# Kernel tuning notes

Hardware: AMD Instinct MI355X
Metric: run time of the kernel (lower is better)

The kernel has to match this reference:

```python
import jax, jax.numpy as jnp
import numpy as np

B, N, FIN, H, D = 2, 512, 128, 4, 64
NEG_SLOPE = 0.2


def setup_inputs() -> dict:
    key = jax.random.key(0)
    ks = jax.random.split(key, 5)
    x = jax.random.normal(ks[0], (B, N, FIN), dtype=jnp.float32)
    # xavier-ish scaled params
    W_proj = jax.random.normal(ks[1], (H, FIN, D), dtype=jnp.float32) * (1.0 / np.sqrt(FIN + D))
    b_proj = jnp.zeros((H, D), dtype=jnp.float32)
    W_cat_weight = jax.random.normal(ks[2], (H, D, 2 * D), dtype=jnp.float32) * (1.0 / np.sqrt(3 * D))
    W_cat_bias = jnp.zeros((H, D), dtype=jnp.float32)
    a = jax.random.normal(ks[3], (H, D), dtype=jnp.float32) * (1.0 / np.sqrt(D))
    bias_param = jnp.zeros((H * D,), dtype=jnp.float32)
    return {"x": x, "W_proj": W_proj, "b_proj": b_proj,
            "W_cat_weight": W_cat_weight, "W_cat_bias": W_cat_bias,
            "a": a, "bias_param": bias_param}


def reference(x, W_proj, b_proj, W_cat_weight, W_cat_bias, a, bias_param):
    # h[b,h,n,d] = W^h x_n + b^h
    h = jnp.einsum('bni,hid->bhnd', x, W_proj) + b_proj[None, :, None, :]
    d = h.shape[-1]
    # W_cat [h_i || h_j] == W1 h_i + W2 h_j  (avoids O(N^2*2D) concat tensor)
    W1 = W_cat_weight[:, :, :d]   # (H, D, D) acts on source node i
    W2 = W_cat_weight[:, :, d:]   # (H, D, D) acts on target node j
    zi = jnp.einsum('bhnd,hed->bhne', h, W1)  # (B,H,N,D)
    zj = jnp.einsum('bhnd,hed->bhne', h, W2)  # (B,H,N,D)
    # z[b,h,i,j,e] = zi[b,h,i,e] + zj[b,h,j,e] + bias, then LeakyReLU
    z = zi[:, :, :, None, :] + zj[:, :, None, :, :] + W_cat_bias[None, :, None, None, :]
    z = jnp.where(z >= 0, z, NEG_SLOPE * z)
    # e[b,h,i,j] = a_h . z
    e = jnp.einsum('bhije,he->bhij', z, a)
    attn = jax.nn.softmax(e, axis=-1)          # softmax over neighbors j
    out = jnp.einsum('bhij,bhjd->bhid', attn, h)  # (B,H,N,D)
    b_, h_, n_, d_ = out.shape
    out = out.transpose(0, 2, 1, 3).reshape(b_, n_, h_ * d_)  # concat heads
    out = out + bias_param
    return out
```

## Files before the change

kernel.cpp:

```cpp
#include <hip/hip_runtime.h>
#include <hip/hip_bf16.h>

#define NN 512
#define FIN 128
#define HH 4
#define DD 64
#define SW 68


__global__ __launch_bounds__(256) void proj_kernel(
    const float* __restrict__ x, const float* __restrict__ Wp,
    const float* __restrict__ bp, const float* __restrict__ Wc,
    const float* __restrict__ Wcb, const float* __restrict__ a,
    float* __restrict__ h_ws, float* __restrict__ azi_ws, float* __restrict__ azj_ws,
    float* __restrict__ adi_ws, float* __restrict__ adj_ws)
{
    int blk = blockIdx.x;
    int bh = blk >> 6;
    int n0 = (blk & 63) << 3;
    int b = bh >> 2, hh = bh & 3;

    __shared__ float xs[8 * FIN];
    __shared__ float hs[8][DD];
    __shared__ float Wcs[DD][2 * DD + 1];

    int t = threadIdx.x;

    ((float4*)xs)[t] = ((const float4*)(x + ((size_t)b * NN + n0) * FIN))[t];
    {
        const float4* wg = (const float4*)(Wc + (size_t)hh * DD * 2 * DD);
        #pragma unroll
        for (int k = 0; k < 8; ++k) {
            int idx = t + 256 * k;
            int r = idx >> 5, c4 = (idx & 31) * 4;
            float4 v = wg[idx];
            Wcs[r][c4] = v.x; Wcs[r][c4 + 1] = v.y;
            Wcs[r][c4 + 2] = v.z; Wcs[r][c4 + 3] = v.w;
        }
    }
    __syncthreads();

    int e = t & 63, w = t >> 6;
    const float* Wph = Wp + (size_t)hh * FIN * DD;
    float bpv = bp[hh * DD + e];
    float acc0 = bpv, acc1 = bpv;
    #pragma unroll 8
    for (int i = 0; i < FIN; ++i) {
        float wv = Wph[i * DD + e];
        acc0 = fmaf(xs[w * FIN + i], wv, acc0);
        acc1 = fmaf(xs[(w + 4) * FIN + i], wv, acc1);
    }
    hs[w][e] = acc0; hs[w + 4][e] = acc1;
    float* hg = h_ws + ((size_t)bh * NN + n0) * DD;
    hg[w * DD + e] = acc0; hg[(w + 4) * DD + e] = acc1;
    __syncthreads();

    float zb = Wcb[hh * DD + e];
    float zi0 = zb, zi1 = zb, zj0 = 0.f, zj1 = 0.f;
    #pragma unroll 8
    for (int d2 = 0; d2 < DD; ++d2) {
        float w1 = Wcs[e][d2];
        float w2 = Wcs[e][DD + d2];
        float h0 = hs[w][d2], h1 = hs[w + 4][d2];
        zi0 = fmaf(h0, w1, zi0); zi1 = fmaf(h1, w1, zi1);
        zj0 = fmaf(h0, w2, zj0); zj1 = fmaf(h1, w2, zj1);
    }

    float av = a[hh * DD + e];
    float p0 = av * zi0, p1 = av * zi1, q0 = av * zj0, q1 = av * zj1;
    #pragma unroll
    for (int off = 32; off; off >>= 1) {
        p0 += __shfl_xor(p0, off); p1 += __shfl_xor(p1, off);
        q0 += __shfl_xor(q0, off); q1 += __shfl_xor(q1, off);
    }
    if (e == 0) {
        adi_ws[bh * NN + n0 + w]     = 0.6f * p0;
        adi_ws[bh * NN + n0 + w + 4] = 0.6f * p1;
        adj_ws[bh * NN + n0 + w]     = 0.6f * q0;
        adj_ws[bh * NN + n0 + w + 4] = 0.6f * q1;
    }

    unsigned long long mask = __ballot(av >= 0.f);
    int np = __popcll(mask);
    int GP = (np + 3) >> 2;
    int below = __popcll(mask & ((1ull << e) - 1ull));
    int slot = (av >= 0.f) ? below : (4 * GP + (e - below));
    float pav = __builtin_fabsf(av);

    float* azib = azi_ws + ((size_t)bh * NN + n0) * SW;
    float* azjb = azj_ws + ((size_t)bh * NN + n0) * SW;
    azib[w * SW + slot]       = pav * zi0;
    azib[(w + 4) * SW + slot] = pav * zi1;
    azjb[w * SW + slot]       = pav * zj0;
    azjb[(w + 4) * SW + slot] = pav * zj1;
    int p1c = 4 * GP - np;
    if (e < 4) {
        int psl = (e < p1c) ? (np + e) : (4 * GP + 64 - np + (e - p1c));
        azib[w * SW + psl] = 0.f; azib[(w + 4) * SW + psl] = 0.f;
        azjb[w * SW + psl] = 0.f; azjb[(w + 4) * SW + psl] = 0.f;
    }
}

__global__ __launch_bounds__(256) void attn_kernel(
    const float* __restrict__ h_ws, const float* __restrict__ azi_ws,
    const float* __restrict__ azj_ws, const float* __restrict__ adi_ws,
    const float* __restrict__ adj_ws, const float* __restrict__ a,
    float* __restrict__ pacc, float* __restrict__ pm, float* __restrict__ ps)
{
    int blk = blockIdx.x;
    int js = blk & 7, it = (blk >> 3) & 63, bh = blk >> 9;
    int j0 = js << 6, i0 = it << 3, hh = bh & 3;

    __shared__ float azis[8 * SW];
    __shared__ float pbuf[8][64];
    __shared__ float htile[64 * 64];

    int t = threadIdx.x, lane = t & 63;
    int w = t >> 6;

    if (t < 136)
        ((float4*)azis)[t] = ((const float4*)(azi_ws + ((size_t)bh * NN + i0) * SW))[t];
    {
        const float4* hsrc = (const float4*)(h_ws + ((size_t)bh * NN + j0) * DD);
        float4* hdst = (float4*)htile;
        #pragma unroll
        for (int k = 0; k < 4; ++k) hdst[t + 256 * k] = hsrc[t + 256 * k];
    }

    float4 azj[17];
    {
        const float4* srcj = (const float4*)(azj_ws + ((size_t)bh * NN + j0 + lane) * SW);
        #pragma unroll
        for (int k = 0; k < 17; ++k) azj[k] = srcj[k];
    }
    float adjv = adj_ws[bh * NN + j0 + lane];

    float av_e = a[hh * DD + lane];
    unsigned long long mask = __ballot(av_e >= 0.f);
    int GP = (__popcll(mask) + 3) >> 2;
    float sgn[17];
    #pragma unroll
    for (int k = 0; k < 17; ++k) sgn[k] = (k < GP) ? 0.4f : -0.4f;

    float adiA = adi_ws[bh * NN + i0 + 2 * w];
    float adiB = adi_ws[bh * NN + i0 + 2 * w + 1];

    __syncthreads();

    #pragma unroll
    for (int ii = 0; ii < 2; ++ii) {
        int i = 2 * w + ii;
        const float4* arow = (const float4*)(azis + i * SW);
        float acc0 = 0.f, acc1 = 0.f;
        #pragma unroll
        for (int k = 0; k < 17; ++k) {
            float4 zi4 = arow[k];
            float s = sgn[k];
            acc0 = fmaf(s, __builtin_fabsf(zi4.x + azj[k].x), acc0);
            acc1 = fmaf(s, __builtin_fabsf(zi4.y + azj[k].y), acc1);
            acc0 = fmaf(s, __builtin_fabsf(zi4.z + azj[k].z), acc0);
            acc1 = fmaf(s, __builtin_fabsf(zi4.w + azj[k].w), acc1);
        }
        float ev = ((ii == 0) ? adiA : adiB) + adjv + acc0 + acc1;
        float m = ev;
        #pragma unroll
        for (int off = 32; off; off >>= 1) m = fmaxf(m, __shfl_xor(m, off));
        float p = __expf(ev - m);
        float ssum = p;
        #pragma unroll
        for (int off = 32; off; off >>= 1) ssum += __shfl_xor(ssum, off);
        pbuf[i][lane] = p;
        if (lane == 0) {
            pm[(js * 8 + bh) * NN + i0 + i] = m;
            ps[(js * 8 + bh) * NN + i0 + i] = ssum;
        }
    }

    float accA = 0.f, accB = 0.f;
    const float4* pA = (const float4*)pbuf[2 * w];
    const float4* pB = (const float4*)pbuf[2 * w + 1];
    #pragma unroll
    for (int k = 0; k < 16; ++k) {
        float4 a4 = pA[k], b4 = pB[k];
        float h0 = htile[(4 * k + 0) * 64 + lane];
        float h1 = htile[(4 * k + 1) * 64 + lane];
        float h2 = htile[(4 * k + 2) * 64 + lane];
        float h3 = htile[(4 * k + 3) * 64 + lane];
        accA = fmaf(a4.x, h0, accA); accB = fmaf(b4.x, h0, accB);
        accA = fmaf(a4.y, h1, accA); accB = fmaf(b4.y, h1, accB);
        accA = fmaf(a4.z, h2, accA); accB = fmaf(b4.z, h2, accB);
        accA = fmaf(a4.w, h3, accA); accB = fmaf(b4.w, h3, accB);
    }
    size_t ob = ((size_t)(js * 8 + bh) * NN + i0 + 2 * w) * DD + lane;
    pacc[ob] = accA;
    pacc[ob + DD] = accB;
}

__global__ __launch_bounds__(256) void combine_kernel(
    const float* __restrict__ pacc, const float* __restrict__ pm,
    const float* __restrict__ ps, const float* __restrict__ bias_param,
    float* __restrict__ out)
{
    int tid = blockIdx.x * 256 + threadIdx.x;
    int d = tid & 63;
    int row = tid >> 6;
    int bh = row >> 9, n = row & 511;
    int b = bh >> 2, hh = bh & 3;
    float mv[8];
    float m = -1e30f;
    #pragma unroll
    for (int p = 0; p < 8; ++p) { mv[p] = pm[p * 4096 + row]; m = fmaxf(m, mv[p]); }
    float denom = 0.f, acc = 0.f;
    #pragma unroll
    for (int p = 0; p < 8; ++p) {
        float wgt = __expf(mv[p] - m);
        denom = fmaf(ps[p * 4096 + row], wgt, denom);
        acc = fmaf(pacc[(size_t)p * 262144 + (size_t)row * 64 + d], wgt, acc);
    }
    out[((size_t)b * NN + n) * (HH * DD) + hh * DD + d] =
        acc / denom + bias_param[hh * DD + d];
}

extern "C" void kernel_launch(void* const* d_in, const int* in_sizes, int n_in,
                              void* d_out, int out_size, void* d_ws, size_t ws_size,
                              hipStream_t stream) {
    const float* x    = (const float*)d_in[0];
    const float* Wp   = (const float*)d_in[1];
    const float* bp   = (const float*)d_in[2];
    const float* Wc   = (const float*)d_in[3];
    const float* Wcb  = (const float*)d_in[4];
    const float* a    = (const float*)d_in[5];
    const float* bpar = (const float*)d_in[6];
    float* out = (float*)d_out;

    float* ws     = (float*)d_ws;
    float* h_ws   = ws;
    float* azi_ws = ws + 262144;
    float* azj_ws = ws + 540672;
    float* adi_ws = ws + 819200;
    float* adj_ws = ws + 823296;
    float* pacc   = ws + 827392;
    float* pm     = ws + 2924544;
    float* ps     = ws + 2957312;

    proj_kernel<<<dim3(512), dim3(256), 0, stream>>>(
        x, Wp, bp, Wc, Wcb, a, h_ws, azi_ws, azj_ws, adi_ws, adj_ws);
    attn_kernel<<<dim3(4096), dim3(256), 0, stream>>>(
        h_ws, azi_ws, azj_ws, adi_ws, adj_ws, a, pacc, pm, ps);
    combine_kernel<<<dim3(1024), dim3(256), 0, stream>>>(
        pacc, pm, ps, bpar, out);
}
```

Baseline: 44.75 us.

## Restructure attention kernel to one row per thread with register-held scores

The attention kernel now gives each thread a source row i, keeps its azi vector and 32 scores in registers, and reads azj and h rows through wave-uniform (broadcast) loads, with no cross-lane shuffle reductions. The j dimension is split into 16 chunks of 32 instead of 8 of 64, so the combine kernel merges 16 partials and the workspace grows. The aim is to drop the shuffle-based softmax and shared-memory staging, at the cost of heavy register pressure (17 float4, 32 scores, 16 float4 accumulators), only 1024 single-wave blocks, and twice the partial-sum traffic.

```diff
diff --git a/kernel.cpp b/kernel.cpp
--- a/kernel.cpp
+++ b/kernel.cpp
@@ -101,99 +101,90 @@
     }
 }
 
-__global__ __launch_bounds__(256) void attn_kernel(
+__global__ __launch_bounds__(64) void attn4(
     const float* __restrict__ h_ws, const float* __restrict__ azi_ws,
     const float* __restrict__ azj_ws, const float* __restrict__ adi_ws,
     const float* __restrict__ adj_ws, const float* __restrict__ a,
     float* __restrict__ pacc, float* __restrict__ pm, float* __restrict__ ps)
 {
     int blk = blockIdx.x;
-    int js = blk & 7, it = (blk >> 3) & 63, bh = blk >> 9;
-    int j0 = js << 6, i0 = it << 3, hh = bh & 3;
-
-    __shared__ float azis[8 * SW];
-    __shared__ float pbuf[8][64];
-    __shared__ float htile[64 * 64];
-
-    int t = threadIdx.x, lane = t & 63;
-    int w = t >> 6;
-
-    if (t < 136)
-        ((float4*)azis)[t] = ((const float4*)(azi_ws + ((size_t)bh * NN + i0) * SW))[t];
+    int js = blk & 15, is_ = (blk >> 4) & 7, bh = blk >> 7;
+    int i0 = is_ << 6, j0 = js << 5, hh = bh & 3;
+    int lane = threadIdx.x;
+
+    __shared__ float tr[64 * 65];
+
+    float4 azi4[17];
     {
-        const float4* hsrc = (const float4*)(h_ws + ((size_t)bh * NN + j0) * DD);
-        float4* hdst = (float4*)htile;
-        #pragma unroll
-        for (int k = 0; k < 4; ++k) hdst[t + 256 * k] = hsrc[t + 256 * k];
-    }
-
-    float4 azj[17];
-    {
-        const float4* srcj = (const float4*)(azj_ws + ((size_t)bh * NN + j0 + lane) * SW);
-        #pragma unroll
-        for (int k = 0; k < 17; ++k) azj[k] = srcj[k];
-    }
-    float adjv = adj_ws[bh * NN + j0 + lane];
+        const float4* zr = (const float4*)(azi_ws + ((size_t)bh * NN + i0 + lane) * SW);
+        #pragma unroll
+        for (int k = 0; k < 17; ++k) azi4[k] = zr[k];
+    }
+    float adiv = adi_ws[bh * NN + i0 + lane];
 
     float av_e = a[hh * DD + lane];
     unsigned long long mask = __ballot(av_e >= 0.f);
     int GP = (__popcll(mask) + 3) >> 2;
-    float sgn[17];
-    #pragma unroll
-    for (int k = 0; k < 17; ++k) sgn[k] = (k < GP) ? 0.4f : -0.4f;
-
-    float adiA = adi_ws[bh * NN + i0 + 2 * w];
-    float adiB = adi_ws[bh * NN + i0 + 2 * w + 1];
-
+
+    const float* ajbase = azj_ws + ((size_t)bh * NN + j0) * SW;
+    const float* adjb   = adj_ws + bh * NN + j0;
+    float p[32];
+
+    #pragma unroll
+    for (int j = 0; j < 32; ++j) {
+        const float4* aj4 = (const float4*)(ajbase + j * SW);
+        float c0 = 0.f, c1 = 0.f, c2 = 0.f, c3 = 0.f;
+        #pragma unroll
+        for (int k = 0; k < 17; ++k) {
+            float4 s4 = aj4[k];
+            float sg = (k < GP) ? 0.4f : -0.4f;
+            c0 = fmaf(sg, __builtin_fabsf(azi4[k].x + s4.x), c0);
+            c1 = fmaf(sg, __builtin_fabsf(azi4[k].y + s4.y), c1);
+            c2 = fmaf(sg, __builtin_fabsf(azi4[k].z + s4.z), c2);
+            c3 = fmaf(sg, __builtin_fabsf(azi4[k].w + s4.w), c3);
+        }
+        p[j] = adiv + adjb[j] + ((c0 + c1) + (c2 + c3));
+    }
+
+    float m = p[0];
+    #pragma unroll
+    for (int j = 1; j < 32; ++j) m = fmaxf(m, p[j]);
+    float s = 0.f;
+    #pragma unroll
+    for (int j = 0; j < 32; ++j) { p[j] = __expf(p[j] - m); s += p[j]; }
+    pm[js * 4096 + bh * NN + i0 + lane] = m;
+    ps[js * 4096 + bh * NN + i0 + lane] = s;
+
+    float4 acc4[16];
+    #pragma unroll
+    for (int k = 0; k < 16; ++k) acc4[k] = make_float4(0.f, 0.f, 0.f, 0.f);
+    const float* hb = h_ws + ((size_t)bh * NN + j0) * DD;
+    #pragma unroll
+    for (int j = 0; j < 32; ++j) {
+        const float4* h4 = (const float4*)(hb + j * DD);
+        float pj = p[j];
+        #pragma unroll
+        for (int k = 0; k < 16; ++k) {
+            float4 hv = h4[k];
+            acc4[k].x = fmaf(pj, hv.x, acc4[k].x);
+            acc4[k].y = fmaf(pj, hv.y, acc4[k].y);
+            acc4[k].z = fmaf(pj, hv.z, acc4[k].z);
+            acc4[k].w = fmaf(pj, hv.w, acc4[k].w);
+        }
+    }
+
+    #pragma unroll
+    for (int k = 0; k < 16; ++k) {
+        tr[lane * 65 + 4 * k + 0] = acc4[k].x;
+        tr[lane * 65 + 4 * k + 1] = acc4[k].y;
+        tr[lane * 65 + 4 * k + 2] = acc4[k].z;
+        tr[lane * 65 + 4 * k + 3] = acc4[k].w;
+    }
     __syncthreads();
-
-    #pragma unroll
-    for (int ii = 0; ii < 2; ++ii) {
-        int i = 2 * w + ii;
-        const float4* arow = (const float4*)(azis + i * SW);
-        float acc0 = 0.f, acc1 = 0.f;
-        #pragma unroll
-        for (int k = 0; k < 17; ++k) {
-            float4 zi4 = arow[k];
-            float s = sgn[k];
-            acc0 = fmaf(s, __builtin_fabsf(zi4.x + azj[k].x), acc0);
-            acc1 = fmaf(s, __builtin_fabsf(zi4.y + azj[k].y), acc1);
-            acc0 = fmaf(s, __builtin_fabsf(zi4.z + azj[k].z), acc0);
-            acc1 = fmaf(s, __builtin_fabsf(zi4.w + azj[k].w), acc1);
-        }
-        float ev = ((ii == 0) ? adiA : adiB) + adjv + acc0 + acc1;
-        float m = ev;
-        #pragma unroll
-        for (int off = 32; off; off >>= 1) m = fmaxf(m, __shfl_xor(m, off));
-        float p = __expf(ev - m);
-        float ssum = p;
-        #pragma unroll
-        for (int off = 32; off; off >>= 1) ssum += __shfl_xor(ssum, off);
-        pbuf[i][lane] = p;
-        if (lane == 0) {
-            pm[(js * 8 + bh) * NN + i0 + i] = m;
-            ps[(js * 8 + bh) * NN + i0 + i] = ssum;
-        }
-    }
-
-    float accA = 0.f, accB = 0.f;
-    const float4* pA = (const float4*)pbuf[2 * w];
-    const float4* pB = (const float4*)pbuf[2 * w + 1];
-    #pragma unroll
-    for (int k = 0; k < 16; ++k) {
-        float4 a4 = pA[k], b4 = pB[k];
-        float h0 = htile[(4 * k + 0) * 64 + lane];
-        float h1 = htile[(4 * k + 1) * 64 + lane];
-        float h2 = htile[(4 * k + 2) * 64 + lane];
-        float h3 = htile[(4 * k + 3) * 64 + lane];
-        accA = fmaf(a4.x, h0, accA); accB = fmaf(b4.x, h0, accB);
-        accA = fmaf(a4.y, h1, accA); accB = fmaf(b4.y, h1, accB);
-        accA = fmaf(a4.z, h2, accA); accB = fmaf(b4.z, h2, accB);
-        accA = fmaf(a4.w, h3, accA); accB = fmaf(b4.w, h3, accB);
-    }
-    size_t ob = ((size_t)(js * 8 + bh) * NN + i0 + 2 * w) * DD + lane;
-    pacc[ob] = accA;
-    pacc[ob + DD] = accB;
+    float* pb = pacc + ((size_t)(js * 8 + bh) * NN + i0) * DD + lane;
+    #pragma unroll
+    for (int i = 0; i < 64; ++i)
+        pb[(size_t)i * DD] = tr[i * 65 + lane];
 }
 
 __global__ __launch_bounds__(256) void combine_kernel(
@@ -206,13 +197,13 @@
     int row = tid >> 6;
     int bh = row >> 9, n = row & 511;
     int b = bh >> 2, hh = bh & 3;
-    float mv[8];
+    float mv[16];
     float m = -1e30f;
     #pragma unroll
-    for (int p = 0; p < 8; ++p) { mv[p] = pm[p * 4096 + row]; m = fmaxf(m, mv[p]); }
+    for (int p = 0; p < 16; ++p) { mv[p] = pm[p * 4096 + row]; m = fmaxf(m, mv[p]); }
     float denom = 0.f, acc = 0.f;
     #pragma unroll
-    for (int p = 0; p < 8; ++p) {
+    for (int p = 0; p < 16; ++p) {
         float wgt = __expf(mv[p] - m);
         denom = fmaf(ps[p * 4096 + row], wgt, denom);
         acc = fmaf(pacc[(size_t)p * 262144 + (size_t)row * 64 + d], wgt, acc);
@@ -240,12 +231,12 @@
     float* adi_ws = ws + 819200;
     float* adj_ws = ws + 823296;
     float* pacc   = ws + 827392;
-    float* pm     = ws + 2924544;
-    float* ps     = ws + 2957312;
+    float* pm     = ws + 5021696;
+    float* ps     = ws + 5087232;
 
     proj_kernel<<<dim3(512), dim3(256), 0, stream>>>(
         x, Wp, bp, Wc, Wcb, a, h_ws, azi_ws, azj_ws, adi_ws, adj_ws);
-    attn_kernel<<<dim3(4096), dim3(256), 0, stream>>>(
+    attn4<<<dim3(1024), dim3(64), 0, stream>>>(
         h_ws, azi_ws, azj_ws, adi_ws, adj_ws, a, pacc, pm, ps);
     combine_kernel<<<dim3(1024), dim3(256), 0, stream>>>(
         pacc, pm, ps, bpar, out);
```

Result: slower. 72.79 us (+62.7%).
